# Performance work log

Hardware: AMD Instinct MI355X
Metric: run time of the kernel (lower is better)

The kernel has to match this reference:

```python
import jax, jax.numpy as jnp
import numpy as np


def _ln(x, g, b, eps=1e-5):
    m = x.mean(-1, keepdims=True)
    v = ((x - m) ** 2).mean(-1, keepdims=True)
    return (x - m) * jax.lax.rsqrt(v + eps) * g + b


def setup_inputs() -> dict:
    key = jax.random.key(0)
    ks = jax.random.split(key, 12)
    B, N, C, D, H, S = 32, 4096, 768, 64, 128, 7
    r = lambda k, shp: jax.random.normal(k, shp, jnp.float32) * 0.02
    return dict(
        x=jax.random.normal(ks[0], (B, N, C), jnp.float32),
        slots=jax.random.normal(ks[1], (B, S, D), jnp.float32),
        g_in=jnp.ones((C,), jnp.float32), b_in=jnp.zeros((C,), jnp.float32),
        g_sl=jnp.ones((D,), jnp.float32), b_sl=jnp.zeros((D,), jnp.float32),
        g_mlp=jnp.ones((D,), jnp.float32), b_mlp=jnp.zeros((D,), jnp.float32),
        Wq=r(ks[2], (D, D)),          # [in, out] layout; y = x @ W
        Wk=r(ks[3], (C, D)),
        Wv=r(ks[4], (C, D)),
        W_ih=r(ks[5], (D, 3 * D)),    # GRUCell input weights, gate order r,z,n
        W_hh=r(ks[6], (D, 3 * D)),
        b_ih=jnp.zeros((3 * D,), jnp.float32),
        b_hh=jnp.zeros((3 * D,), jnp.float32),
        w1=r(ks[7], (D, H)), bb1=jnp.zeros((H,), jnp.float32),
        w2=r(ks[8], (H, D)), bb2=jnp.zeros((D,), jnp.float32),
        num_iters=3,
    )


def reference(x, slots, g_in, b_in, g_sl, b_sl, g_mlp, b_mlp,
              Wq, Wk, Wv, W_ih, W_hh, b_ih, b_hh, w1, bb1, w2, bb2,
              num_iters):
    D = slots.shape[-1]
    scale = D ** -0.5
    xn = _ln(x, g_in, b_in)              # BNC
    k = xn @ Wk                          # BND
    v = xn @ Wv                          # BND
    weights = None
    for _ in range(num_iters):
        q = _ln(slots, g_sl, b_sl) @ Wq  # BSD
        logits = jnp.einsum('bsd,bnd->bsn', q, k) * scale
        # inverted attention: softmax over slots (queries)
        weights = jax.nn.softmax(logits, axis=1)               # BSN
        wn = weights / (weights.sum(-1, keepdims=True) + 1e-8)  # weighted mean over N
        attn = jnp.einsum('bsn,bnd->bsd', wn, v)               # BSD
        # GRUCell(input=attn, hidden=slots), PyTorch semantics
        gi = attn @ W_ih + b_ih
        gh = slots @ W_hh + b_hh
        ir, iz, in_ = jnp.split(gi, 3, axis=-1)
        hr, hz, hn = jnp.split(gh, 3, axis=-1)
        r = jax.nn.sigmoid(ir + hr)
        z = jax.nn.sigmoid(iz + hz)
        n = jnp.tanh(in_ + r * hn)
        slots = (1.0 - z) * n + z * slots
        # residual MLP
        slots = slots + (jax.nn.relu(_ln(slots, g_mlp, b_mlp) @ w1 + bb1) @ w2 + bb2)
    return slots, weights
```

## Files before the change

### kernel.cpp

```cpp
#include <hip/hip_runtime.h>
#include <hip/hip_bf16.h>
#include <math.h>


typedef __bf16 bf16x8 __attribute__((ext_vector_type(8)));
typedef float  f32x4  __attribute__((ext_vector_type(4)));
typedef unsigned short u16x8 __attribute__((ext_vector_type(8)));

#define NB 32
#define NN 4096
#define NC 768
#define ND 64
#define NS 7

__device__ __forceinline__ float wave_sum64(float v) {
#pragma unroll
  for (int o = 32; o > 0; o >>= 1) v += __shfl_xor(v, o, 64);
  return v;
}

__device__ __forceinline__ float bf2f(unsigned short u) {
  union { unsigned int i; float f; } c;
  c.i = ((unsigned int)u) << 16;
  return c.f;
}

__device__ __forceinline__ void glds16(const void* g, void* l) {
  __builtin_amdgcn_global_load_lds(
      (const __attribute__((address_space(1))) unsigned int*)(uintptr_t)g,
      (__attribute__((address_space(3))) unsigned int*)(unsigned int)(uintptr_t)l,
      16, 0, 0);
}

__device__ __forceinline__ void slots_ln_q(float h, int t, const float* g_sl,
                                           const float* b_sl, const float* Wq,
                                           float* y_s, float* q_out) {
  float m = wave_sum64(h) * (1.0f / 64.0f);
  float dx = h - m;
  float var = wave_sum64(dx * dx) * (1.0f / 64.0f);
  float rstd = rsqrtf(var + 1e-5f);
  y_s[t] = dx * rstd * g_sl[t] + b_sl[t];
  __syncthreads();
  float q = 0.f;
#pragma unroll 8
  for (int i = 0; i < 64; ++i) q = fmaf(y_s[i], Wq[i * 64 + t], q);
  q_out[t] = q;
}

__global__ __launch_bounds__(64) void k_prep(
    const float* __restrict__ Wk, const float* __restrict__ Wv,
    const float* __restrict__ g_in, const float* __restrict__ b_in,
    const float* __restrict__ slots_in, const float* __restrict__ g_sl,
    const float* __restrict__ b_sl, const float* __restrict__ Wq,
    __bf16* __restrict__ GWt, float* __restrict__ GWsum, float* __restrict__ BW,
    float* __restrict__ slots_ws, float* __restrict__ q_ws,
    float* __restrict__ num, float* __restrict__ den) {
  __shared__ float y_s[64];
  int t = threadIdx.x;
  int bid = blockIdx.x;
  if (bid < 128) {
    int d = bid;
    const float* W = (d < 64) ? (Wk + d) : (Wv + (d - 64));
    float sgw = 0.f, sbw = 0.f;
    for (int j = 0; j < 12; ++j) {
      int c = t + 64 * j;
      float w = W[(size_t)c * 64];
      float gw = g_in[c] * w;
      GWt[(size_t)d * NC + c] = (__bf16)gw;
      sgw += gw;
      sbw += b_in[c] * w;
    }
    sgw = wave_sum64(sgw);
    sbw = wave_sum64(sbw);
    if (t == 0) { GWsum[d] = sgw; BW[d] = sbw; }
  } else {
    int bs = bid - 128;
    float h = slots_in[bs * 64 + t];
    slots_ws[bs * 64 + t] = h;
    num[bs * 64 + t] = 0.f;
    if (t == 0) den[bs] = 0.f;
    slots_ln_q(h, t, g_sl, b_sl, Wq, y_s, q_ws + bs * 64);
  }
}

#define BM 128
#define LDA 72

__global__ __launch_bounds__(256) void k_gemm_kv(
    const float* __restrict__ x, const __bf16* __restrict__ GWt,
    const float* __restrict__ GWsum, const float* __restrict__ BW,
    __bf16* __restrict__ kbuf, __bf16* __restrict__ vbuf) {
  __shared__ __bf16 As[BM * LDA] __attribute__((aligned(16)));
  __shared__ __bf16 Bs[128 * 64] __attribute__((aligned(16)));
  __shared__ float mean_s[128], rstd_s[128], gws_s[128], bw_s[128];

  int t = threadIdx.x;
  int blk = blockIdx.x;
  int lane = t & 63, wave = t >> 6;
  int wr = wave >> 1, wc = wave & 1;
  int grp = lane >> 4, lr = lane & 15;
  int r = t >> 1, half = t & 1;

  if (t < 128) { gws_s[t] = GWsum[t]; bw_s[t] = BW[t]; }

  f32x4 acc[4][4] = {};
  float s1 = 0.f, s2 = 0.f;

  const float* xrow = x + (size_t)(blk * BM + r) * NC + half * 32;
  const char* gB = (const char*)GWt + (size_t)(wave * 32 + (lane >> 3)) * (NC * 2) +
                   (lane & 7) * 16;
  char* lB = (char*)&Bs[0] + wave * 4096;

  for (int ck = 0; ck < 12; ++ck) {
    __syncthreads();
#pragma unroll
    for (int j = 0; j < 4; ++j)
      glds16(gB + ck * 128 + j * 8 * (NC * 2), lB + j * 1024);
    {
      const float4* p4 = (const float4*)(xrow + ck * 64);
      __bf16* dst = &As[r * LDA + half * 32];
#pragma unroll
      for (int j = 0; j < 4; ++j) {
        float4 a = p4[2 * j], b = p4[2 * j + 1];
        bf16x8 pk;
        pk[0] = (__bf16)a.x; pk[1] = (__bf16)a.y; pk[2] = (__bf16)a.z; pk[3] = (__bf16)a.w;
        pk[4] = (__bf16)b.x; pk[5] = (__bf16)b.y; pk[6] = (__bf16)b.z; pk[7] = (__bf16)b.w;
        s1 += (a.x + a.y + a.z + a.w) + (b.x + b.y + b.z + b.w);
        s2 += a.x * a.x + a.y * a.y + a.z * a.z + a.w * a.w +
              b.x * b.x + b.y * b.y + b.z * b.z + b.w * b.w;
        *(bf16x8*)(dst + j * 8) = pk;
      }
    }
    __syncthreads();
#pragma unroll
    for (int kk = 0; kk < 2; ++kk) {
      bf16x8 af[4], bfr[4];
#pragma unroll
      for (int i = 0; i < 4; ++i)
        af[i] = *(const bf16x8*)&As[(wr * 64 + i * 16 + lr) * LDA + kk * 32 + grp * 8];
#pragma unroll
      for (int i = 0; i < 4; ++i)
        bfr[i] = *(const bf16x8*)&Bs[(wc * 64 + i * 16 + lr) * 64 + kk * 32 + grp * 8];
#pragma unroll
      for (int i = 0; i < 4; ++i)
#pragma unroll
        for (int j = 0; j < 4; ++j)
          acc[i][j] = __builtin_amdgcn_mfma_f32_16x16x32_bf16(af[i], bfr[j], acc[i][j], 0, 0, 0);
    }
  }

  s1 += __shfl_xor(s1, 1, 64);
  s2 += __shfl_xor(s2, 1, 64);
  if (half == 0) {
    float m = s1 * (1.0f / 768.0f);
    float var = s2 * (1.0f / 768.0f) - m * m;
    mean_s[r] = m;
    rstd_s[r] = rsqrtf(var + 1e-5f);
  }
  __syncthreads();

#pragma unroll
  for (int i = 0; i < 4; ++i) {
#pragma unroll
    for (int j = 0; j < 4; ++j) {
      int colb = wc * 64 + j * 16 + lr;
      float gw = gws_s[colb], bw = bw_s[colb];
      __bf16* obuf = (colb < 64) ? kbuf : vbuf;
      int ocol = colb & 63;
#pragma unroll
      for (int e = 0; e < 4; ++e) {
        int row = wr * 64 + i * 16 + grp * 4 + e;
        float rs = rstd_s[row], m = mean_s[row];
        float val = rs * acc[i][j][e] - m * rs * gw + bw;
        obuf[(size_t)(blk * BM + row) * 64 + ocol] = (__bf16)val;
      }
    }
  }
}

__global__ __launch_bounds__(256) void k_attn(
    const __bf16* __restrict__ kbuf, const __bf16* __restrict__ vbuf,
    const float* __restrict__ q_ws, float* __restrict__ out_w,
    float* __restrict__ num, float* __restrict__ den, int write_w) {
  __shared__ float q_s[7 * 64];
  __shared__ float w_s[7 * 130];
  __shared__ float v_s[128 * 68] __attribute__((aligned(16)));
  __shared__ float den_p[28];
  __shared__ float red[7 * 4 * 64];

  int t = threadIdx.x;
  int b = blockIdx.x >> 5;
  int n0 = (blockIdx.x & 31) * 128;

  for (int idx = t; idx < 448; idx += 256) q_s[idx] = q_ws[b * 448 + idx];
  __syncthreads();

  int nl = t >> 1, dh = t & 1;
  float kf[32];
  {
    const u16x8* kp = (const u16x8*)(kbuf + ((size_t)b * NN + n0 + nl) * 64 + dh * 32);
#pragma unroll
    for (int j = 0; j < 4; ++j) {
      u16x8 a = kp[j];
#pragma unroll
      for (int m = 0; m < 8; ++m) kf[j * 8 + m] = bf2f(a[m]);
    }
  }

  float lg[7];
#pragma unroll
  for (int s = 0; s < 7; ++s) {
    const float* qv = &q_s[s * 64 + dh * 32];
    float d0 = 0.f;
#pragma unroll
    for (int j = 0; j < 32; ++j) d0 = fmaf(kf[j], qv[j], d0);
    d0 += __shfl_xor(d0, 1, 64);
    lg[s] = d0 * 0.125f;
  }
  float mx = lg[0];
#pragma unroll
  for (int s = 1; s < 7; ++s) mx = fmaxf(mx, lg[s]);
  float sum = 0.f;
#pragma unroll
  for (int s = 0; s < 7; ++s) { lg[s] = __expf(lg[s] - mx); sum += lg[s]; }
  float inv = 1.0f / sum;
  if (dh == 0) {
#pragma unroll
    for (int s = 0; s < 7; ++s) w_s[s * 130 + nl] = lg[s] * inv;
  }
  __syncthreads();

  if (write_w) {
    for (int idx = t; idx < 896; idx += 256) {
      int s = idx >> 7, n = idx & 127;
      out_w[(size_t)b * 7 * NN + (size_t)s * NN + n0 + n] = w_s[s * 130 + n];
    }
  }
  if (t < 28) {
    int s = t >> 2, qq = t & 3;
    float ds = 0.f;
    for (int j = 0; j < 32; ++j) ds += w_s[s * 130 + qq * 32 + j];
    den_p[t] = ds;
  }
  {
    const u16x8* vp = (const u16x8*)(vbuf + ((size_t)b * NN + n0 + nl) * 64 + dh * 32);
    float4* dst = (float4*)&v_s[nl * 68 + dh * 32];
#pragma unroll
    for (int j = 0; j < 4; ++j) {
      u16x8 a = vp[j];
      float4 lo = {bf2f(a[0]), bf2f(a[1]), bf2f(a[2]), bf2f(a[3])};
      float4 hi = {bf2f(a[4]), bf2f(a[5]), bf2f(a[6]), bf2f(a[7])};
      dst[2 * j] = lo;
      dst[2 * j + 1] = hi;
    }
  }
  __syncthreads();
  if (t < 7)
    atomicAdd(&den[b * 7 + t],
              den_p[4 * t] + den_p[4 * t + 1] + den_p[4 * t + 2] + den_p[4 * t + 3]);

  int d = t & 63, qtr = t >> 6;
  float np_[7] = {0, 0, 0, 0, 0, 0, 0};
  for (int j = 0; j < 32; ++j) {
    int n = qtr * 32 + j;
    float vv = v_s[n * 68 + d];
#pragma unroll
    for (int s = 0; s < 7; ++s) np_[s] = fmaf(w_s[s * 130 + n], vv, np_[s]);
  }
#pragma unroll
  for (int s = 0; s < 7; ++s) red[(s * 4 + qtr) * 64 + d] = np_[s];
  __syncthreads();
  for (int idx = t; idx < 448; idx += 256) {
    int s = idx >> 6, dd = idx & 63;
    float sm = red[(s * 4 + 0) * 64 + dd] + red[(s * 4 + 1) * 64 + dd] +
               red[(s * 4 + 2) * 64 + dd] + red[(s * 4 + 3) * 64 + dd];
    atomicAdd(&num[(b * 7 + s) * 64 + dd], sm);
  }
}

__global__ __launch_bounds__(64) void k_gru(
    float* __restrict__ num, float* __restrict__ den,
    float* __restrict__ slots_ws, const float* __restrict__ W_ih,
    const float* __restrict__ W_hh, const float* __restrict__ b_ih,
    const float* __restrict__ b_hh, const float* __restrict__ w1,
    const float* __restrict__ bb1, const float* __restrict__ w2,
    const float* __restrict__ bb2, const float* __restrict__ g_mlp,
    const float* __restrict__ b_mlp, const float* __restrict__ g_sl,
    const float* __restrict__ b_sl, const float* __restrict__ Wq,
    float* __restrict__ q_ws, float* __restrict__ out_slots) {
  __shared__ float att_s[64], h_s[64], y_s[64], a_s[128];
  int t = threadIdx.x;
  int bs = blockIdx.x;

  float h = slots_ws[bs * 64 + t];
  float dn = den[bs];
  float at = num[bs * 64 + t] / (dn + 1e-8f);
  att_s[t] = at;
  h_s[t] = h;
  __syncthreads();
  num[bs * 64 + t] = 0.f;
  if (t == 0) den[bs] = 0.f;

  float gi0 = b_ih[t], gi1 = b_ih[64 + t], gi2 = b_ih[128 + t];
  float gh0 = b_hh[t], gh1 = b_hh[64 + t], gh2 = b_hh[128 + t];
#pragma unroll 4
  for (int i = 0; i < 64; ++i) {
    float ai = att_s[i], hi = h_s[i];
    const float* wi = W_ih + i * 192 + t;
    const float* wh = W_hh + i * 192 + t;
    gi0 = fmaf(ai, wi[0], gi0);
    gi1 = fmaf(ai, wi[64], gi1);
    gi2 = fmaf(ai, wi[128], gi2);
    gh0 = fmaf(hi, wh[0], gh0);
    gh1 = fmaf(hi, wh[64], gh1);
    gh2 = fmaf(hi, wh[128], gh2);
  }
  float rr = 1.f / (1.f + __expf(-(gi0 + gh0)));
  float zz = 1.f / (1.f + __expf(-(gi1 + gh1)));
  float nn = tanhf(gi2 + rr * gh2);
  float hn = (1.f - zz) * nn + zz * h;

  float m = wave_sum64(hn) * (1.f / 64.f);
  float dx = hn - m;
  float var = wave_sum64(dx * dx) * (1.f / 64.f);
  float rstd = rsqrtf(var + 1e-5f);
  y_s[t] = dx * rstd * g_mlp[t] + b_mlp[t];
  __syncthreads();
  float a0 = bb1[t], a1 = bb1[64 + t];
#pragma unroll 4
  for (int i = 0; i < 64; ++i) {
    float yi = y_s[i];
    a0 = fmaf(yi, w1[i * 128 + t], a0);
    a1 = fmaf(yi, w1[i * 128 + 64 + t], a1);
  }
  a_s[t] = fmaxf(a0, 0.f);
  a_s[64 + t] = fmaxf(a1, 0.f);
  __syncthreads();
  float o = hn + bb2[t];
#pragma unroll 4
  for (int j = 0; j < 128; ++j) o = fmaf(a_s[j], w2[j * 64 + t], o);

  slots_ws[bs * 64 + t] = o;
  out_slots[bs * 64 + t] = o;
  __syncthreads();
  slots_ln_q(o, t, g_sl, b_sl, Wq, y_s, q_ws + bs * 64);
}

extern "C" void kernel_launch(void* const* d_in, const int* in_sizes, int n_in,
                              void* d_out, int out_size, void* d_ws, size_t ws_size,
                              hipStream_t stream) {
  const float* x      = (const float*)d_in[0];
  const float* slots  = (const float*)d_in[1];
  const float* g_in   = (const float*)d_in[2];
  const float* b_in   = (const float*)d_in[3];
  const float* g_sl   = (const float*)d_in[4];
  const float* b_sl   = (const float*)d_in[5];
  const float* g_mlp  = (const float*)d_in[6];
  const float* b_mlp  = (const float*)d_in[7];
  const float* Wq     = (const float*)d_in[8];
  const float* Wk     = (const float*)d_in[9];
  const float* Wv     = (const float*)d_in[10];
  const float* W_ih   = (const float*)d_in[11];
  const float* W_hh   = (const float*)d_in[12];
  const float* b_ih   = (const float*)d_in[13];
  const float* b_hh   = (const float*)d_in[14];
  const float* w1     = (const float*)d_in[15];
  const float* bb1    = (const float*)d_in[16];
  const float* w2     = (const float*)d_in[17];
  const float* bb2    = (const float*)d_in[18];

  float* out_slots = (float*)d_out;
  float* out_w     = (float*)d_out + (size_t)NB * NS * ND;

  char* ws = (char*)d_ws;
  __bf16* GWt      = (__bf16*)(ws);
  float*  GWsum    = (float*)(ws + 196608);
  float*  BW       = (float*)(ws + 197120);
  float*  q_ws     = (float*)(ws + 197632);
  float*  num      = (float*)(ws + 254976);
  float*  den      = (float*)(ws + 312320);
  float*  slots_ws = (float*)(ws + 313344);
  __bf16* kbuf     = (__bf16*)(ws + 370688);
  __bf16* vbuf     = (__bf16*)(ws + 370688 + 16777216);
  (void)ws_size; (void)in_sizes; (void)n_in; (void)out_size;

  k_prep<<<352, 64, 0, stream>>>(Wk, Wv, g_in, b_in, slots, g_sl, b_sl, Wq,
                                 GWt, GWsum, BW, slots_ws, q_ws, num, den);
  k_gemm_kv<<<1024, 256, 0, stream>>>(x, GWt, GWsum, BW, kbuf, vbuf);
  for (int it = 0; it < 3; ++it) {
    k_attn<<<1024, 256, 0, stream>>>(kbuf, vbuf, q_ws, out_w, num, den,
                                     it == 2 ? 1 : 0);
    k_gru<<<224, 64, 0, stream>>>(num, den, slots_ws, W_ih, W_hh, b_ih, b_hh,
                                  w1, bb1, w2, bb2, g_mlp, b_mlp, g_sl, b_sl,
                                  Wq, q_ws, out_slots);
  }
}
```

Measured before the change: 699.0 us.

## Fuse first attention iteration into K/V projection GEMM epilogue

The K/V GEMM kernel now keeps its bf16 output tile in shared memory and runs the first iteration's slot logits, softmax over slots, denominator and weighted-V numerator accumulation directly from it. The first standalone attention launch is removed, so K and V are not re-read from global memory for that iteration. Shared memory is unioned with the GEMM staging buffers, which raises per-block LDS use and may reduce occupancy of the GEMM.

```diff
diff --git a/kernel.cpp b/kernel.cpp
--- a/kernel.cpp
+++ b/kernel.cpp
@@ -85,23 +85,39 @@
 
 #define BM 128
 #define LDA 72
+#define LDKV 136
 
 __global__ __launch_bounds__(256) void k_gemm_kv(
     const float* __restrict__ x, const __bf16* __restrict__ GWt,
     const float* __restrict__ GWsum, const float* __restrict__ BW,
-    __bf16* __restrict__ kbuf, __bf16* __restrict__ vbuf) {
-  __shared__ __bf16 As[BM * LDA] __attribute__((aligned(16)));
-  __shared__ __bf16 Bs[128 * 64] __attribute__((aligned(16)));
-  __shared__ float mean_s[128], rstd_s[128], gws_s[128], bw_s[128];
+    const float* __restrict__ q_ws, __bf16* __restrict__ kbuf,
+    __bf16* __restrict__ vbuf, float* __restrict__ num,
+    float* __restrict__ den) {
+  __shared__ char smem[2048 + 34816 + 3640 + 112 + 7168 + 1792]
+      __attribute__((aligned(16)));
+  float* mean_s = (float*)smem;
+  float* rstd_s = (float*)(smem + 512);
+  float* gws_s  = (float*)(smem + 1024);
+  float* bw_s   = (float*)(smem + 1536);
+  __bf16* As    = (__bf16*)(smem + 2048);
+  __bf16* Bs    = (__bf16*)(smem + 2048 + 18432);
+  __bf16* kv_s  = (__bf16*)(smem + 2048);
+  float* w_s    = (float*)(smem + 2048 + 34816);
+  float* den_p  = (float*)(smem + 2048 + 34816 + 3640);
+  float* red_s  = (float*)(smem + 2048 + 34816 + 3640 + 112);
+  float* q_s    = (float*)(smem + 2048 + 34816 + 3640 + 112 + 7168);
 
   int t = threadIdx.x;
   int blk = blockIdx.x;
+  int b = blk >> 5;
+  int n0 = (blk & 31) * 128;
   int lane = t & 63, wave = t >> 6;
   int wr = wave >> 1, wc = wave & 1;
   int grp = lane >> 4, lr = lane & 15;
   int r = t >> 1, half = t & 1;
 
   if (t < 128) { gws_s[t] = GWsum[t]; bw_s[t] = BW[t]; }
+  for (int idx = t; idx < 448; idx += 256) q_s[idx] = q_ws[b * 448 + idx];
 
   f32x4 acc[4][4] = {};
   float s1 = 0.f, s2 = 0.f;
@@ -121,13 +137,13 @@
       __bf16* dst = &As[r * LDA + half * 32];
 #pragma unroll
       for (int j = 0; j < 4; ++j) {
-        float4 a = p4[2 * j], b = p4[2 * j + 1];
+        float4 a = p4[2 * j], bb = p4[2 * j + 1];
         bf16x8 pk;
         pk[0] = (__bf16)a.x; pk[1] = (__bf16)a.y; pk[2] = (__bf16)a.z; pk[3] = (__bf16)a.w;
-        pk[4] = (__bf16)b.x; pk[5] = (__bf16)b.y; pk[6] = (__bf16)b.z; pk[7] = (__bf16)b.w;
-        s1 += (a.x + a.y + a.z + a.w) + (b.x + b.y + b.z + b.w);
+        pk[4] = (__bf16)bb.x; pk[5] = (__bf16)bb.y; pk[6] = (__bf16)bb.z; pk[7] = (__bf16)bb.w;
+        s1 += (a.x + a.y + a.z + a.w) + (bb.x + bb.y + bb.z + bb.w);
         s2 += a.x * a.x + a.y * a.y + a.z * a.z + a.w * a.w +
-              b.x * b.x + b.y * b.y + b.z * b.z + b.w * b.w;
+              bb.x * bb.x + bb.y * bb.y + bb.z * bb.z + bb.w * bb.w;
         *(bf16x8*)(dst + j * 8) = pk;
       }
     }
@@ -171,10 +187,75 @@
       for (int e = 0; e < 4; ++e) {
         int row = wr * 64 + i * 16 + grp * 4 + e;
         float rs = rstd_s[row], m = mean_s[row];
-        float val = rs * acc[i][j][e] - m * rs * gw + bw;
-        obuf[(size_t)(blk * BM + row) * 64 + ocol] = (__bf16)val;
+        __bf16 val = (__bf16)(rs * acc[i][j][e] - m * rs * gw + bw);
+        obuf[(size_t)(blk * BM + row) * 64 + ocol] = val;
+        kv_s[row * LDKV + colb] = val;
       }
     }
+  }
+  __syncthreads();
+
+  int nl = t >> 1, dh = t & 1;
+  float kf[32];
+  {
+    const u16x8* kp = (const u16x8*)&kv_s[nl * LDKV + dh * 32];
+#pragma unroll
+    for (int j = 0; j < 4; ++j) {
+      u16x8 a = kp[j];
+#pragma unroll
+      for (int m = 0; m < 8; ++m) kf[j * 8 + m] = bf2f(a[m]);
+    }
+  }
+  float lg[7];
+#pragma unroll
+  for (int s = 0; s < 7; ++s) {
+    const float* qv = &q_s[s * 64 + dh * 32];
+    float d0 = 0.f;
+#pragma unroll
+    for (int j = 0; j < 32; ++j) d0 = fmaf(kf[j], qv[j], d0);
+    d0 += __shfl_xor(d0, 1, 64);
+    lg[s] = d0 * 0.125f;
+  }
+  float mx = lg[0];
+#pragma unroll
+  for (int s = 1; s < 7; ++s) mx = fmaxf(mx, lg[s]);
+  float sum = 0.f;
+#pragma unroll
+  for (int s = 0; s < 7; ++s) { lg[s] = __expf(lg[s] - mx); sum += lg[s]; }
+  float inv = 1.0f / sum;
+  if (dh == 0) {
+#pragma unroll
+    for (int s = 0; s < 7; ++s) w_s[s * 130 + nl] = lg[s] * inv;
+  }
+  __syncthreads();
+
+  if (t < 28) {
+    int s = t >> 2, qq = t & 3;
+    float ds = 0.f;
+    for (int j = 0; j < 32; ++j) ds += w_s[s * 130 + qq * 32 + j];
+    den_p[t] = ds;
+  }
+  __syncthreads();
+  if (t < 7)
+    atomicAdd(&den[b * 7 + t],
+              den_p[4 * t] + den_p[4 * t + 1] + den_p[4 * t + 2] + den_p[4 * t + 3]);
+
+  int d = t & 63, qtr = t >> 6;
+  float np_[7] = {0, 0, 0, 0, 0, 0, 0};
+  for (int j = 0; j < 32; ++j) {
+    int n = qtr * 32 + j;
+    float vv = bf2f(*(const unsigned short*)&kv_s[n * LDKV + 64 + d]);
+#pragma unroll
+    for (int s = 0; s < 7; ++s) np_[s] = fmaf(w_s[s * 130 + n], vv, np_[s]);
+  }
+#pragma unroll
+  for (int s = 0; s < 7; ++s) red_s[(s * 4 + qtr) * 64 + d] = np_[s];
+  __syncthreads();
+  for (int idx = t; idx < 448; idx += 256) {
+    int s = idx >> 6, dd = idx & 63;
+    float sm = red_s[(s * 4 + 0) * 64 + dd] + red_s[(s * 4 + 1) * 64 + dd] +
+               red_s[(s * 4 + 2) * 64 + dd] + red_s[(s * 4 + 3) * 64 + dd];
+    atomicAdd(&num[(b * 7 + s) * 64 + dd], sm);
   }
 }
 
@@ -386,8 +467,12 @@
 
   k_prep<<<352, 64, 0, stream>>>(Wk, Wv, g_in, b_in, slots, g_sl, b_sl, Wq,
                                  GWt, GWsum, BW, slots_ws, q_ws, num, den);
-  k_gemm_kv<<<1024, 256, 0, stream>>>(x, GWt, GWsum, BW, kbuf, vbuf);
-  for (int it = 0; it < 3; ++it) {
+  k_gemm_kv<<<1024, 256, 0, stream>>>(x, GWt, GWsum, BW, q_ws, kbuf, vbuf,
+                                      num, den);
+  k_gru<<<224, 64, 0, stream>>>(num, den, slots_ws, W_ih, W_hh, b_ih, b_hh,
+                                w1, bb1, w2, bb2, g_mlp, b_mlp, g_sl, b_sl,
+                                Wq, q_ws, out_slots);
+  for (int it = 1; it < 3; ++it) {
     k_attn<<<1024, 256, 0, stream>>>(kbuf, vbuf, q_ws, out_w, num, den,
                                      it == 2 ? 1 : 0);
     k_gru<<<224, 64, 0, stream>>>(num, den, slots_ws, W_ih, W_hh, b_ih, b_hh,
```

Result: no change. 698.9 us (-0.0%).
